# Kernel tuning notes

Hardware: AMD Instinct MI355X
Metric: run time of the kernel (lower is better)

The kernel has to match this reference:

```python
import jax, jax.numpy as jnp
import numpy as np

INNER_LR = 0.01        # inner-loop fast-weight learning rate
ADAPTER_SCALE = 1.0    # adapter_scale from __init__
INIT_STD = 0.001       # init_std for phi_0 fast-weight initialization
VOCAB = 32000


def setup_inputs() -> dict:
    key = jax.random.key(0)
    k1, k2, k3, k4, k5 = jax.random.split(key, 5)
    B, S, H, R, V = 2, 2048, 1024, 16, VOCAB
    hidden_states = jax.random.normal(k1, (B, S, H), dtype=jnp.float32)
    input_ids = jax.random.randint(k2, (B, S), 0, V)
    # phi_0 learned fast-weight initialization (init_std-scaled, per TTTMetaAdapter)
    fast_a = jax.random.normal(k3, (H, R), dtype=jnp.float32) * INIT_STD
    fast_b = jax.random.normal(k4, (R, H), dtype=jnp.float32) * INIT_STD
    lm_head = jax.random.normal(k5, (H, V), dtype=jnp.float32) * 0.02
    return {"hidden_states": hidden_states, "input_ids": input_ids,
            "fast_a": fast_a, "fast_b": fast_b, "lm_head": lm_head}


def _next_token_loss(logits, input_ids):
    # ttt_next_token_loss_from_logits: CE(logits[:, :-1], input_ids[:, 1:])
    logp = jax.nn.log_softmax(logits[:, :-1, :], axis=-1)       # [B, S-1, V]
    tgt = input_ids[:, 1:]                                       # [B, S-1]
    nll = -jnp.take_along_axis(logp, tgt[..., None], axis=-1)[..., 0]
    return nll.mean()


def _apply(hidden_states, a, b):
    # TTTState.apply: h + (h @ fast_a @ fast_b) * scale
    return hidden_states + ((hidden_states @ a) @ b) * ADAPTER_SCALE


def reference(hidden_states, input_ids, fast_a, fast_b, lm_head):
    # Inner objective: next-token CE of adapted hidden states through lm_head.
    def inner_loss(a, b):
        adapted = _apply(hidden_states, a, b)                    # [B, S, H]
        logits = adapted @ lm_head                               # [B, S, V]
        return _next_token_loss(logits, input_ids)

    loss, (ga, gb) = jax.value_and_grad(inner_loss, argnums=(0, 1))(fast_a, fast_b)
    grad_norm = jnp.sqrt(jnp.sum(ga * ga) + jnp.sum(gb * gb))
    # One differentiable TTT inner gradient step on the fast weights.
    new_a = fast_a - INNER_LR * ga
    new_b = fast_b - INNER_LR * gb
    out = _apply(hidden_states, new_a, new_b)                    # adapted output
    return out, new_a, new_b, loss, grad_norm
```

## Files before the change

### kernel.cpp

```cpp
#include <hip/hip_runtime.h>
#include <hip/hip_bf16.h>


#define ROWS 4096
#define Hdim 1024
#define Rdim 16
#define Vdim 32000
#define NVALID 4094.0f
#define LRATE 0.01f
#define RB 32
#define VT 512
#define LAS 1032

typedef __attribute__((ext_vector_type(8))) short bf16x8;
typedef __attribute__((ext_vector_type(4))) float f32x4;

static __device__ __forceinline__ float bf2f(short u) {
  union { float f; unsigned int i; } w; w.i = ((unsigned int)(unsigned short)u) << 16; return w.f;
}
static __device__ __forceinline__ short f2bf(float f) {
  union { float f; unsigned int i; } w; w.f = f;
  unsigned int lsb = (w.i >> 16) & 1u;
  w.i += 0x7fffu + lsb;
  return (short)(w.i >> 16);
}
static __device__ __forceinline__ f32x4 mfma16(bf16x8 a, bf16x8 b, f32x4 c) {
  return __builtin_amdgcn_mfma_f32_16x16x32_bf16(a, b, c, 0, 0, 0);
}
static __device__ __forceinline__ f32x4 mfma8(long a, long b, f32x4 c) {
  return __builtin_amdgcn_mfma_f32_16x16x32_fp8_fp8(a, b, c, 0, 0, 0);
}
static __device__ __forceinline__ int pk4fp8(float f0, float f1, float f2, float f3) {
  int v = __builtin_amdgcn_cvt_pk_fp8_f32(f0, f1, 0, false);
  v = __builtin_amdgcn_cvt_pk_fp8_f32(f2, f3, v, true);
  return v;
}

#define OFF_BP2   ((size_t)0)
#define OFF_BP1   ((size_t)65536000)
#define OFF_ADP   ((size_t)98304000)
#define OFF_ADP8  ((size_t)106692608)
#define OFF_DA    ((size_t)110886912)
#define OFF_U     ((size_t)127664128)
#define OFF_DU    ((size_t)127926272)
#define OFF_Z     ((size_t)128188416)
#define OFF_GA    ((size_t)128221184)
#define OFF_GB    ((size_t)128286720)
#define OFF_LOSS  ((size_t)128352256)

#define OUT_A    ((size_t)4194304)
#define OUT_B    ((size_t)4210688)
#define OUT_LOSS ((size_t)4227072)
#define OUT_GN   ((size_t)4227073)

__global__ void k_pack(const float* __restrict__ in, char* __restrict__ Bp1,
                       short* __restrict__ Bp2) {
  __shared__ float tile[32][260];
  int v0 = blockIdx.x * 256, k0 = blockIdx.y * 32;
  int tid = threadIdx.x;
#pragma unroll
  for (int r = 0; r < 32; ++r)
    tile[r][tid] = in[(size_t)(k0 + r) * Vdim + v0 + tid];
  __syncthreads();
  int lane = tid & 63, l15 = lane & 15, q = (lane >> 4) & 3, g = tid >> 6;
#pragma unroll
  for (int it = 0; it < 4; ++it) {
    int vbl = it * 4 + g;
    float f[8];
#pragma unroll
    for (int j = 0; j < 8; ++j) f[j] = tile[q * 8 + j][vbl * 16 + l15];
    int2 w2;
    w2.x = pk4fp8(f[0], f[1], f[2], f[3]);
    w2.y = pk4fp8(f[4], f[5], f[6], f[7]);
    *(int2*)(Bp1 + ((size_t)(v0 / 16 + vbl) * 32 + k0 / 32) * 512 + lane * 8) = w2;
  }
#pragma unroll
  for (int it = 0; it < 4; ++it) {
    int idx = it * 4 + g;
    int hbl = idx >> 3, vkbl = idx & 7;
    bf16x8 frag;
#pragma unroll
    for (int j = 0; j < 8; ++j) frag[j] = f2bf(tile[hbl * 16 + l15][vkbl * 32 + q * 8 + j]);
    *(bf16x8*)(Bp2 + ((size_t)(k0 / 16 + hbl) * 1000 + v0 / 32 + vkbl) * 512 + lane * 8) = frag;
  }
}

__global__ void k_prep_ua(const float* __restrict__ hs, const float* __restrict__ fa,
                          const float* __restrict__ fb, float* __restrict__ u,
                          short* __restrict__ adp, char* __restrict__ adp8) {
  __shared__ float wred[4][16];
  __shared__ float ubc[16];
  int row = blockIdx.x, tid = threadIdx.x, lane = tid & 63, w = tid >> 6;
  const float* hrow = hs + (size_t)row * Hdim;
  float4 hv = *(const float4*)(hrow + tid * 4);
  float ur[16];
  const float* fap = fa + (size_t)tid * 4 * Rdim;
#pragma unroll
  for (int r = 0; r < 16; ++r)
    ur[r] = hv.x * fap[r] + hv.y * fap[16 + r] + hv.z * fap[32 + r] + hv.w * fap[48 + r];
#pragma unroll
  for (int r = 0; r < 16; ++r)
#pragma unroll
    for (int off = 32; off; off >>= 1) ur[r] += __shfl_xor(ur[r], off);
  if (lane == 0) {
#pragma unroll
    for (int r = 0; r < 16; ++r) wred[w][r] = ur[r];
  }
  __syncthreads();
  if (tid < 16) {
    float s = wred[0][tid] + wred[1][tid] + wred[2][tid] + wred[3][tid];
    ubc[tid] = s;
    u[row * Rdim + tid] = s;
  }
  __syncthreads();
  float a0 = hv.x, a1 = hv.y, a2 = hv.z, a3 = hv.w;
#pragma unroll
  for (int r = 0; r < 16; ++r) {
    float uv = ubc[r];
    float4 bv = *(const float4*)(fb + r * Hdim + tid * 4);
    a0 += uv * bv.x; a1 += uv * bv.y; a2 += uv * bv.z; a3 += uv * bv.w;
  }
  short4 o; o.x = f2bf(a0); o.y = f2bf(a1); o.z = f2bf(a2); o.w = f2bf(a3);
  *(short4*)(adp + (size_t)row * Hdim + tid * 4) = o;
  *(int*)(adp8 + (size_t)row * Hdim + tid * 4) = pk4fp8(a0, a1, a2, a3);
}

__launch_bounds__(1024, 4)
__global__ void k_fused(const char* __restrict__ adp8, const char* __restrict__ Bp1,
                        const short* __restrict__ Bp2, short* __restrict__ dApart,
                        float* __restrict__ zpart) {
  __shared__ __align__(16) char lA[RB * LAS];
  __shared__ __align__(16) short lP[2][RB * VT];
  __shared__ float zred[RB * 16];
  int tid = threadIdx.x, lane = tid & 63, w = tid >> 6;
  int q = lane >> 4, l15 = lane & 15;
  int L = blockIdx.x;
  int sp = (L >> 2) & 1;
  int rg = (L & 3) | ((L >> 3) << 2);
  int row0 = rg * RB;
  int v0beg = sp ? 15872 : 0;
  int v0end = sp ? 32000 : 15872;
  int nt = sp ? 32 : 31;

#pragma unroll
  for (int i = 0; i < 4; ++i) {
    int idx = tid + i * 1024;
    int r = idx >> 7, kk8 = (idx & 127) * 8;
    *(int2*)(lA + r * LAS + kk8) = *(const int2*)(adp8 + (size_t)(row0 + r) * Hdim + kk8);
  }
  if (tid < RB * 16) zred[tid] = 0.f;

  f32x4 acc[2][4];
#pragma unroll
  for (int rf = 0; rf < 2; ++rf)
#pragma unroll
    for (int cf = 0; cf < 4; ++cf)
#pragma unroll
      for (int i = 0; i < 4; ++i) acc[rf][cf][i] = 0.f;

  __syncthreads();

  for (int t = 0; t < nt; ++t) {
    int v0 = v0beg + t * VT;
    int rem = v0end - v0; if (rem > VT) rem = VT;
    char* lPc = (char*)lP[t & 1];
    f32x4 lacc[2][2];
#pragma unroll
    for (int rf = 0; rf < 2; ++rf)
#pragma unroll
      for (int cf = 0; cf < 2; ++cf)
#pragma unroll
        for (int i = 0; i < 4; ++i) lacc[rf][cf][i] = 0.f;
#pragma unroll 8
    for (int ks = 0; ks < 32; ++ks) {
      int kk = ks * 32 + q * 8;
      long af[2], bfr[2];
      af[0] = *(const long*)(lA + l15 * LAS + kk);
      af[1] = *(const long*)(lA + (16 + l15) * LAS + kk);
#pragma unroll
      for (int cf = 0; cf < 2; ++cf) {
        int vb = v0 / 16 + w * 2 + cf;
        if (vb > 1999) vb = 1999;
        bfr[cf] = *(const long*)(Bp1 + ((size_t)vb * 32 + ks) * 512 + lane * 8);
      }
#pragma unroll
      for (int rf = 0; rf < 2; ++rf)
#pragma unroll
        for (int cf = 0; cf < 2; ++cf)
          lacc[rf][cf] = mfma8(af[rf], bfr[cf], lacc[rf][cf]);
    }
#pragma unroll
    for (int rf = 0; rf < 2; ++rf)
#pragma unroll
      for (int i = 0; i < 4; ++i) {
        int r = rf * 16 + q * 4 + i;
        float z = 0.f;
#pragma unroll
        for (int cf = 0; cf < 2; ++cf) {
          int c0 = w * 32 + cf * 16;
          float pv = (c0 < rem) ? __expf(lacc[rf][cf][i]) : 0.f;
          z += pv;
          int c = c0 + l15;
          *(short*)(lPc + r * 1024 + ((c * 2) ^ ((r & 7) << 4))) = f2bf(pv);
        }
#pragma unroll
        for (int off = 1; off < 16; off <<= 1) z += __shfl_xor(z, off);
        if (l15 == 0) zred[r * 16 + w] += z;
      }
    __syncthreads();
#pragma unroll 4
    for (int ks = 0; ks < 16; ++ks) {
      int kb = ks * 32 + q * 8;
      int vkb = v0 / 32 + ks;
      if (vkb > 999) vkb = 999;
      bf16x8 pa[2], bg[4];
#pragma unroll
      for (int rf = 0; rf < 2; ++rf) {
        int r = rf * 16 + l15;
        pa[rf] = *(const bf16x8*)(lPc + r * 1024 + ((kb * 2) ^ ((r & 7) << 4)));
      }
#pragma unroll
      for (int cf = 0; cf < 4; ++cf)
        bg[cf] = *(const bf16x8*)(Bp2 + ((size_t)(w * 4 + cf) * 1000 + vkb) * 512 + lane * 8);
#pragma unroll
      for (int rf = 0; rf < 2; ++rf)
#pragma unroll
        for (int cf = 0; cf < 4; ++cf)
          acc[rf][cf] = mfma16(pa[rf], bg[cf], acc[rf][cf]);
    }
  }
  __syncthreads();
  if (tid < RB) {
    float z = 0.f;
#pragma unroll
    for (int g = 0; g < 16; ++g) z += zred[tid * 16 + g];
    zpart[sp * ROWS + row0 + tid] = z;
  }
#pragma unroll
  for (int rf = 0; rf < 2; ++rf)
#pragma unroll
    for (int cf = 0; cf < 4; ++cf)
#pragma unroll
      for (int i = 0; i < 4; ++i) {
        int r = rf * 16 + q * 4 + i;
        int h = w * 64 + cf * 16 + l15;
        dApart[((size_t)(row0 + r) * 2 + sp) * Hdim + h] = f2bf(acc[rf][cf][i]);
      }
}

__global__ void k_post_du(const short* __restrict__ adp, const short* __restrict__ Bp2,
                          const float* __restrict__ fb, const int* __restrict__ ids,
                          const float* __restrict__ zpart, char* __restrict__ dAx,
                          float* __restrict__ du, float* __restrict__ loss_acc) {
  __shared__ float red[256];
  __shared__ float wredu[4][16];
  int row = blockIdx.x, tid = threadIdx.x, lane = tid & 63, w = tid >> 6;
  int b = row >> 11, s = row & 2047;
  bool valid = s < 2047;
  float Z = zpart[row] + zpart[ROWS + row];
  float sc = 1.f / (Z * NVALID);
  int tgt = valid ? ids[b * 2048 + s + 1] : 0;
  const short* prow = (const short*)(dAx + (size_t)row * 4096);
  short4 p0 = *(const short4*)(prow + tid * 4);
  short4 p1 = *(const short4*)(prow + 1024 + tid * 4);
  short4 a4 = *(const short4*)(adp + (size_t)row * Hdim + tid * 4);
  int tq = (tgt >> 3) & 3, tj = tgt & 7, tvkb = tgt >> 5;
  float lcv[4], d[4];
#pragma unroll
  for (int c = 0; c < 4; ++c) {
    int h = tid * 4 + c;
    short lcs = Bp2[((size_t)(h >> 4) * 1000 + tvkb) * 512 +
                    (size_t)(((h & 15) + 16 * tq) * 8 + tj)];
    lcv[c] = bf2f(lcs);
  }
  float q0[4] = {bf2f(p0.x), bf2f(p0.y), bf2f(p0.z), bf2f(p0.w)};
  float q1[4] = {bf2f(p1.x), bf2f(p1.y), bf2f(p1.z), bf2f(p1.w)};
  float avv[4] = {bf2f(a4.x), bf2f(a4.y), bf2f(a4.z), bf2f(a4.w)};
#pragma unroll
  for (int c = 0; c < 4; ++c)
    d[c] = valid ? ((q0[c] + q1[c]) * sc - lcv[c] * (1.f / NVALID)) : 0.f;
  __syncthreads();
  float* drow = (float*)(dAx + (size_t)row * 4096);
  float dot = 0.f;
#pragma unroll
  for (int c = 0; c < 4; ++c) {
    drow[tid * 4 + c] = d[c];
    dot += avv[c] * lcv[c];
  }
  float pdu[16];
#pragma unroll
  for (int r = 0; r < 16; ++r) {
    float4 bv = *(const float4*)(fb + r * Hdim + tid * 4);
    pdu[r] = d[0] * bv.x + d[1] * bv.y + d[2] * bv.z + d[3] * bv.w;
  }
#pragma unroll
  for (int r = 0; r < 16; ++r)
#pragma unroll
    for (int off = 32; off; off >>= 1) pdu[r] += __shfl_xor(pdu[r], off);
  if (lane == 0) {
#pragma unroll
    for (int r = 0; r < 16; ++r) wredu[w][r] = pdu[r];
  }
  red[tid] = dot;
  __syncthreads();
  if (tid < 16)
    du[row * Rdim + tid] = wredu[0][tid] + wredu[1][tid] + wredu[2][tid] + wredu[3][tid];
  if (!valid) return;
  for (int o = 128; o; o >>= 1) {
    if (tid < o) red[tid] += red[tid + o];
    __syncthreads();
  }
  if (tid == 0) atomicAdd(loss_acc, (logf(Z) - red[0]) / NVALID);
}

__global__ void k_ga_gb(const float* __restrict__ hs, const float* __restrict__ dA,
                        const float* __restrict__ u, const float* __restrict__ du,
                        float* __restrict__ ga, float* __restrict__ gb) {
  __shared__ float lu[512 * 16], ldu[512 * 16];
  int tid = threadIdx.x;
  int h = blockIdx.x * 256 + tid;
  int r0 = blockIdx.y * 512;
#pragma unroll
  for (int i = 0; i < 32; ++i) {
    int idx = tid + i * 256;
    lu[idx] = u[(size_t)r0 * Rdim + idx];
    ldu[idx] = du[(size_t)r0 * Rdim + idx];
  }
  __syncthreads();
  float aga[16], agb[16];
#pragma unroll
  for (int r = 0; r < 16; ++r) { aga[r] = 0.f; agb[r] = 0.f; }
  for (int rl = 0; rl < 512; ++rl) {
    int row = r0 + rl;
    float hv = hs[(size_t)row * Hdim + h];
    float dv = dA[(size_t)row * Hdim + h];
#pragma unroll
    for (int r = 0; r < 16; ++r) {
      aga[r] += hv * ldu[rl * 16 + r];
      agb[r] += lu[rl * 16 + r] * dv;
    }
  }
#pragma unroll
  for (int r = 0; r < 16; ++r) {
    atomicAdd(&ga[h * Rdim + r], aga[r]);
    atomicAdd(&gb[r * Hdim + h], agb[r]);
  }
}

__global__ void k_finalize(const float* __restrict__ fa, const float* __restrict__ fb,
                           const float* __restrict__ ga, const float* __restrict__ gb,
                           const float* __restrict__ loss_acc, float* __restrict__ out) {
  __shared__ float red[512];
  int tid = threadIdx.x;
  float s = 0.f;
  for (int i = tid; i < 32768; i += 512) {
    float g = ga[i];
    s += g * g;
  }
  red[tid] = s; __syncthreads();
  for (int o = 256; o; o >>= 1) {
    if (tid < o) red[tid] += red[tid + o];
    __syncthreads();
  }
  float gn = sqrtf(red[0]);
  for (int i = tid; i < 16384; i += 512) {
    out[OUT_A + i] = fa[i] - LRATE * ga[i];
    out[OUT_B + i] = fb[i] - LRATE * gb[i];
  }
  if (tid == 0) { out[OUT_LOSS] = loss_acc[0]; out[OUT_GN] = gn; }
}

__global__ void k_tail_uo(const float* __restrict__ hs, const float* __restrict__ outAB,
                          float* __restrict__ out) {
  __shared__ float wred[4][16];
  __shared__ float ubc[16];
  int row = blockIdx.x, tid = threadIdx.x, lane = tid & 63, w = tid >> 6;
  const float* na = outAB;
  const float* nb = outAB + 16384;
  const float* hrow = hs + (size_t)row * Hdim;
  float4 hv = *(const float4*)(hrow + tid * 4);
  float ur[16];
  const float* nap = na + (size_t)tid * 4 * Rdim;
#pragma unroll
  for (int r = 0; r < 16; ++r)
    ur[r] = hv.x * nap[r] + hv.y * nap[16 + r] + hv.z * nap[32 + r] + hv.w * nap[48 + r];
#pragma unroll
  for (int r = 0; r < 16; ++r)
#pragma unroll
    for (int off = 32; off; off >>= 1) ur[r] += __shfl_xor(ur[r], off);
  if (lane == 0) {
#pragma unroll
    for (int r = 0; r < 16; ++r) wred[w][r] = ur[r];
  }
  __syncthreads();
  if (tid < 16) ubc[tid] = wred[0][tid] + wred[1][tid] + wred[2][tid] + wred[3][tid];
  __syncthreads();
  float a0 = hv.x, a1 = hv.y, a2 = hv.z, a3 = hv.w;
#pragma unroll
  for (int r = 0; r < 16; ++r) {
    float uv = ubc[r];
    float4 bv = *(const float4*)(nb + r * Hdim + tid * 4);
    a0 += uv * bv.x; a1 += uv * bv.y; a2 += uv * bv.z; a3 += uv * bv.w;
  }
  float4 o; o.x = a0; o.y = a1; o.z = a2; o.w = a3;
  *(float4*)(out + (size_t)row * Hdim + tid * 4) = o;
}

extern "C" void kernel_launch(void* const* d_in, const int* in_sizes, int n_in,
                              void* d_out, int out_size, void* d_ws, size_t ws_size,
                              hipStream_t stream) {
  (void)in_sizes; (void)n_in; (void)out_size; (void)ws_size;
  const float* hs   = (const float*)d_in[0];
  const int*   ids  = (const int*)d_in[1];
  const float* fa   = (const float*)d_in[2];
  const float* fb   = (const float*)d_in[3];
  const float* lmhf = (const float*)d_in[4];
  float* out = (float*)d_out;
  char* ws = (char*)d_ws;

  short* Bp2    = (short*)(ws + OFF_BP2);
  char*  Bp1    = ws + OFF_BP1;
  short* adp    = (short*)(ws + OFF_ADP);
  char*  adp8   = ws + OFF_ADP8;
  char*  dAx    = ws + OFF_DA;
  float* u      = (float*)(ws + OFF_U);
  float* du     = (float*)(ws + OFF_DU);
  float* zpart  = (float*)(ws + OFF_Z);
  float* ga     = (float*)(ws + OFF_GA);
  float* gb     = (float*)(ws + OFF_GB);
  float* loss_acc = (float*)(ws + OFF_LOSS);

  hipMemsetAsync(ws + OFF_GA, 0, 65536 * 2 + 4, stream);

  k_pack<<<dim3(125, 32), 256, 0, stream>>>(lmhf, Bp1, Bp2);
  k_prep_ua<<<4096, 256, 0, stream>>>(hs, fa, fb, u, adp, adp8);
  k_fused<<<256, 1024, 0, stream>>>(adp8, Bp1, Bp2, (short*)dAx, zpart);
  k_post_du<<<4096, 256, 0, stream>>>(adp, Bp2, fb, ids, zpart, dAx, du, loss_acc);
  k_ga_gb<<<dim3(4, 8), 256, 0, stream>>>(hs, (float*)dAx, u, du, ga, gb);
  k_finalize<<<1, 512, 0, stream>>>(fa, fb, ga, gb, loss_acc, out);
  k_tail_uo<<<4096, 256, 0, stream>>>(hs, out + OUT_A, out);
}
```

Measured before the change: 1.017 ms.

## Add transposed bf16 lm_head, drop bf16 adapted copy, defer Z reduction, raise MFMA priority

k_pack can now also write a row-major bf16 transposed lm_head when the workspace is large enough, so k_post_du reads a contiguous target column instead of scattered Bp2 elements. The bf16 adapted-hidden buffer is removed and k_post_du decodes the fp8 copy instead, which saves a write and a read but lowers precision in the dot product used for the loss. In k_fused the per-tile shuffle reduction of Z is replaced by per-thread register accumulators reduced once at the end, and s_setprio brackets the MFMA loops. The transposed copy adds a 64 MB write to the pack kernel.

```diff
diff --git a/kernel.cpp b/kernel.cpp
--- a/kernel.cpp
+++ b/kernel.cpp
@@ -35,18 +35,28 @@
   v = __builtin_amdgcn_cvt_pk_fp8_f32(f2, f3, v, true);
   return v;
 }
+static __device__ __forceinline__ float fp8tof(char c) {
+  union { float f; unsigned int i; } w;
+  unsigned int u = (unsigned char)c;
+  unsigned int s = (u >> 7) & 1u, e = (u >> 3) & 0xfu, m = u & 7u;
+  if (e == 0) { w.f = (float)m * 0.001953125f; }
+  else { w.i = ((e + 120u) << 23) | (m << 20); }
+  if (s) w.f = -w.f;
+  return w.f;
+}
 
 #define OFF_BP2   ((size_t)0)
 #define OFF_BP1   ((size_t)65536000)
-#define OFF_ADP   ((size_t)98304000)
-#define OFF_ADP8  ((size_t)106692608)
-#define OFF_DA    ((size_t)110886912)
-#define OFF_U     ((size_t)127664128)
-#define OFF_DU    ((size_t)127926272)
-#define OFF_Z     ((size_t)128188416)
-#define OFF_GA    ((size_t)128221184)
-#define OFF_GB    ((size_t)128286720)
-#define OFF_LOSS  ((size_t)128352256)
+#define OFF_ADP8  ((size_t)98304000)
+#define OFF_DA    ((size_t)102498304)
+#define OFF_U     ((size_t)119275520)
+#define OFF_DU    ((size_t)119537664)
+#define OFF_Z     ((size_t)119799808)
+#define OFF_GA    ((size_t)119832576)
+#define OFF_GB    ((size_t)119898112)
+#define OFF_LOSS  ((size_t)119963648)
+#define OFF_LMHT  ((size_t)119963776)
+#define WS_NEED_LMHT (OFF_LMHT + (size_t)65536000)
 
 #define OUT_A    ((size_t)4194304)
 #define OUT_B    ((size_t)4210688)
@@ -54,7 +64,7 @@
 #define OUT_GN   ((size_t)4227073)
 
 __global__ void k_pack(const float* __restrict__ in, char* __restrict__ Bp1,
-                       short* __restrict__ Bp2) {
+                       short* __restrict__ Bp2, short* __restrict__ lmhT) {
   __shared__ float tile[32][260];
   int v0 = blockIdx.x * 256, k0 = blockIdx.y * 32;
   int tid = threadIdx.x;
@@ -83,11 +93,20 @@
     for (int j = 0; j < 8; ++j) frag[j] = f2bf(tile[hbl * 16 + l15][vkbl * 32 + q * 8 + j]);
     *(bf16x8*)(Bp2 + ((size_t)(k0 / 16 + hbl) * 1000 + v0 / 32 + vkbl) * 512 + lane * 8) = frag;
   }
+  if (lmhT) {
+#pragma unroll
+    for (int jj = 0; jj < 4; ++jj) {
+      bf16x8 fr;
+#pragma unroll
+      for (int j = 0; j < 8; ++j) fr[j] = f2bf(tile[jj * 8 + j][tid]);
+      *(bf16x8*)(lmhT + (size_t)(v0 + tid) * 1024 + k0 + jj * 8) = fr;
+    }
+  }
 }
 
 __global__ void k_prep_ua(const float* __restrict__ hs, const float* __restrict__ fa,
                           const float* __restrict__ fb, float* __restrict__ u,
-                          short* __restrict__ adp, char* __restrict__ adp8) {
+                          char* __restrict__ adp8) {
   __shared__ float wred[4][16];
   __shared__ float ubc[16];
   int row = blockIdx.x, tid = threadIdx.x, lane = tid & 63, w = tid >> 6;
@@ -120,8 +139,6 @@
     float4 bv = *(const float4*)(fb + r * Hdim + tid * 4);
     a0 += uv * bv.x; a1 += uv * bv.y; a2 += uv * bv.z; a3 += uv * bv.w;
   }
-  short4 o; o.x = f2bf(a0); o.y = f2bf(a1); o.z = f2bf(a2); o.w = f2bf(a3);
-  *(short4*)(adp + (size_t)row * Hdim + tid * 4) = o;
   *(int*)(adp8 + (size_t)row * Hdim + tid * 4) = pk4fp8(a0, a1, a2, a3);
 }
 
@@ -148,9 +165,11 @@
     int r = idx >> 7, kk8 = (idx & 127) * 8;
     *(int2*)(lA + r * LAS + kk8) = *(const int2*)(adp8 + (size_t)(row0 + r) * Hdim + kk8);
   }
-  if (tid < RB * 16) zred[tid] = 0.f;
-
+
+  float zacc[8];
   f32x4 acc[2][4];
+#pragma unroll
+  for (int j = 0; j < 8; ++j) zacc[j] = 0.f;
 #pragma unroll
   for (int rf = 0; rf < 2; ++rf)
 #pragma unroll
@@ -171,6 +190,7 @@
       for (int cf = 0; cf < 2; ++cf)
 #pragma unroll
         for (int i = 0; i < 4; ++i) lacc[rf][cf][i] = 0.f;
+    __builtin_amdgcn_s_setprio(1);
 #pragma unroll 8
     for (int ks = 0; ks < 32; ++ks) {
       int kk = ks * 32 + q * 8;
@@ -189,25 +209,23 @@
         for (int cf = 0; cf < 2; ++cf)
           lacc[rf][cf] = mfma8(af[rf], bfr[cf], lacc[rf][cf]);
     }
+    __builtin_amdgcn_s_setprio(0);
 #pragma unroll
     for (int rf = 0; rf < 2; ++rf)
 #pragma unroll
       for (int i = 0; i < 4; ++i) {
         int r = rf * 16 + q * 4 + i;
-        float z = 0.f;
 #pragma unroll
         for (int cf = 0; cf < 2; ++cf) {
           int c0 = w * 32 + cf * 16;
           float pv = (c0 < rem) ? __expf(lacc[rf][cf][i]) : 0.f;
-          z += pv;
+          zacc[rf * 4 + i] += pv;
           int c = c0 + l15;
           *(short*)(lPc + r * 1024 + ((c * 2) ^ ((r & 7) << 4))) = f2bf(pv);
         }
-#pragma unroll
-        for (int off = 1; off < 16; off <<= 1) z += __shfl_xor(z, off);
-        if (l15 == 0) zred[r * 16 + w] += z;
       }
     __syncthreads();
+    __builtin_amdgcn_s_setprio(1);
 #pragma unroll 4
     for (int ks = 0; ks < 16; ++ks) {
       int kb = ks * 32 + q * 8;
@@ -228,7 +246,17 @@
         for (int cf = 0; cf < 4; ++cf)
           acc[rf][cf] = mfma16(pa[rf], bg[cf], acc[rf][cf]);
     }
-  }
+    __builtin_amdgcn_s_setprio(0);
+  }
+#pragma unroll
+  for (int rf = 0; rf < 2; ++rf)
+#pragma unroll
+    for (int i = 0; i < 4; ++i) {
+      float z = zacc[rf * 4 + i];
+#pragma unroll
+      for (int off = 1; off < 16; off <<= 1) z += __shfl_xor(z, off);
+      if (l15 == 0) zred[(rf * 16 + q * 4 + i) * 16 + w] = z;
+    }
   __syncthreads();
   if (tid < RB) {
     float z = 0.f;
@@ -248,10 +276,11 @@
       }
 }
 
-__global__ void k_post_du(const short* __restrict__ adp, const short* __restrict__ Bp2,
-                          const float* __restrict__ fb, const int* __restrict__ ids,
-                          const float* __restrict__ zpart, char* __restrict__ dAx,
-                          float* __restrict__ du, float* __restrict__ loss_acc) {
+__global__ void k_post_du(const char* __restrict__ adp8, const short* __restrict__ Bp2,
+                          const short* __restrict__ lmhT, const float* __restrict__ fb,
+                          const int* __restrict__ ids, const float* __restrict__ zpart,
+                          char* __restrict__ dAx, float* __restrict__ du,
+                          float* __restrict__ loss_acc) {
   __shared__ float red[256];
   __shared__ float wredu[4][16];
   int row = blockIdx.x, tid = threadIdx.x, lane = tid & 63, w = tid >> 6;
@@ -263,19 +292,26 @@
   const short* prow = (const short*)(dAx + (size_t)row * 4096);
   short4 p0 = *(const short4*)(prow + tid * 4);
   short4 p1 = *(const short4*)(prow + 1024 + tid * 4);
-  short4 a4 = *(const short4*)(adp + (size_t)row * Hdim + tid * 4);
-  int tq = (tgt >> 3) & 3, tj = tgt & 7, tvkb = tgt >> 5;
-  float lcv[4], d[4];
-#pragma unroll
-  for (int c = 0; c < 4; ++c) {
-    int h = tid * 4 + c;
-    short lcs = Bp2[((size_t)(h >> 4) * 1000 + tvkb) * 512 +
-                    (size_t)(((h & 15) + 16 * tq) * 8 + tj)];
-    lcv[c] = bf2f(lcs);
+  int a8 = *(const int*)(adp8 + (size_t)row * Hdim + tid * 4);
+  float lcv[4];
+  if (lmhT) {
+    short4 lc4 = *(const short4*)(lmhT + (size_t)tgt * 1024 + tid * 4);
+    lcv[0] = bf2f(lc4.x); lcv[1] = bf2f(lc4.y); lcv[2] = bf2f(lc4.z); lcv[3] = bf2f(lc4.w);
+  } else {
+    int tq = (tgt >> 3) & 3, tj = tgt & 7, tvkb = tgt >> 5;
+#pragma unroll
+    for (int c = 0; c < 4; ++c) {
+      int h = tid * 4 + c;
+      short lcs = Bp2[((size_t)(h >> 4) * 1000 + tvkb) * 512 +
+                      (size_t)(((h & 15) + 16 * tq) * 8 + tj)];
+      lcv[c] = bf2f(lcs);
+    }
   }
   float q0[4] = {bf2f(p0.x), bf2f(p0.y), bf2f(p0.z), bf2f(p0.w)};
   float q1[4] = {bf2f(p1.x), bf2f(p1.y), bf2f(p1.z), bf2f(p1.w)};
-  float avv[4] = {bf2f(a4.x), bf2f(a4.y), bf2f(a4.z), bf2f(a4.w)};
+  float avv[4] = {fp8tof((char)(a8 & 0xff)), fp8tof((char)((a8 >> 8) & 0xff)),
+                  fp8tof((char)((a8 >> 16) & 0xff)), fp8tof((char)((a8 >> 24) & 0xff))};
+  float d[4];
 #pragma unroll
   for (int c = 0; c < 4; ++c)
     d[c] = valid ? ((q0[c] + q1[c]) * sc - lcv[c] * (1.f / NVALID)) : 0.f;
@@ -409,7 +445,7 @@
 extern "C" void kernel_launch(void* const* d_in, const int* in_sizes, int n_in,
                               void* d_out, int out_size, void* d_ws, size_t ws_size,
                               hipStream_t stream) {
-  (void)in_sizes; (void)n_in; (void)out_size; (void)ws_size;
+  (void)in_sizes; (void)n_in; (void)out_size;
   const float* hs   = (const float*)d_in[0];
   const int*   ids  = (const int*)d_in[1];
   const float* fa   = (const float*)d_in[2];
@@ -420,7 +456,6 @@
 
   short* Bp2    = (short*)(ws + OFF_BP2);
   char*  Bp1    = ws + OFF_BP1;
-  short* adp    = (short*)(ws + OFF_ADP);
   char*  adp8   = ws + OFF_ADP8;
   char*  dAx    = ws + OFF_DA;
   float* u      = (float*)(ws + OFF_U);
@@ -429,13 +464,14 @@
   float* ga     = (float*)(ws + OFF_GA);
   float* gb     = (float*)(ws + OFF_GB);
   float* loss_acc = (float*)(ws + OFF_LOSS);
+  short* lmhT   = (ws_size >= WS_NEED_LMHT) ? (short*)(ws + OFF_LMHT) : (short*)nullptr;
 
   hipMemsetAsync(ws + OFF_GA, 0, 65536 * 2 + 4, stream);
 
-  k_pack<<<dim3(125, 32), 256, 0, stream>>>(lmhf, Bp1, Bp2);
-  k_prep_ua<<<4096, 256, 0, stream>>>(hs, fa, fb, u, adp, adp8);
+  k_pack<<<dim3(125, 32), 256, 0, stream>>>(lmhf, Bp1, Bp2, lmhT);
+  k_prep_ua<<<4096, 256, 0, stream>>>(hs, fa, fb, u, adp8);
   k_fused<<<256, 1024, 0, stream>>>(adp8, Bp1, Bp2, (short*)dAx, zpart);
-  k_post_du<<<4096, 256, 0, stream>>>(adp, Bp2, fb, ids, zpart, dAx, du, loss_acc);
+  k_post_du<<<4096, 256, 0, stream>>>(adp8, Bp2, lmhT, fb, ids, zpart, dAx, du, loss_acc);
   k_ga_gb<<<dim3(4, 8), 256, 0, stream>>>(hs, (float*)dAx, u, du, ga, gb);
   k_finalize<<<1, 512, 0, stream>>>(fa, fb, ga, gb, loss_acc, out);
   k_tail_uo<<<4096, 256, 0, stream>>>(hs, out + OUT_A, out);
```

Result: slower. 1.228 ms (+20.7%).
